# Kernel optimization log

Hardware: AMD Instinct MI355X
Metric: run time of the kernel (lower is better)

## Reference

```python
import jax, jax.numpy as jnp
import numpy as np
import math

MODEL_DIM = 1024
B, S = 4, 2048


def setup_inputs() -> dict:
    key = jax.random.key(0)
    k_x, k_q, k_k, k_v = jax.random.split(key, 4)
    r5 = math.sqrt(5)
    x = jax.random.normal(k_x, (B, S, MODEL_DIM), dtype=jnp.float32)
    Q = jax.random.uniform(k_q, (MODEL_DIM, MODEL_DIM), minval=-r5, maxval=r5, dtype=jnp.float32)
    K = jax.random.uniform(k_k, (MODEL_DIM, MODEL_DIM), minval=-r5, maxval=r5, dtype=jnp.float32)
    V = jax.random.uniform(k_v, (MODEL_DIM, MODEL_DIM), minval=-r5, maxval=r5, dtype=jnp.float32)
    # attention_input == 'both' -> a == model_dim -> F is the full identity
    F = jnp.eye(MODEL_DIM, dtype=jnp.float32)
    return {"x": x, "Q": Q, "K": K, "V": V, "F": F}


def reference(x, Q, K, V, F):
    d = x.shape[-1]
    xf = jnp.matmul(x, F)
    Qx = jnp.matmul(xf, Q)          # [B,S,D]
    Kx = jnp.matmul(xf, K)          # [B,S,D]
    Vx = jnp.matmul(x, V)           # [B,S,D]
    scores = jnp.einsum('bqd,bkd->bqk', Qx, Kx) / math.sqrt(d)  # [B,S,S]
    seq = x.shape[1]
    mask = jnp.triu(jnp.ones((seq, seq), dtype=bool), k=1)
    scores = jnp.where(mask, -jnp.inf, scores)
    probs = jax.nn.softmax(scores, axis=-1)
    out = jnp.matmul(probs, Vx)     # [B,S,D]
    return (out, probs)
```

## Files before the change

### kernel.cpp

```cpp
#include <hip/hip_runtime.h>
#include <hip/hip_fp16.h>

typedef _Float16 f16;
typedef __attribute__((ext_vector_type(8))) _Float16 f16x8;
typedef __attribute__((ext_vector_type(4))) _Float16 f16x4;
typedef __attribute__((ext_vector_type(4))) float    f32x4;

#define D_MODEL 1024
#define SEQ     2048
#define BATCH   4
#define M_TOT   (BATCH * SEQ)
#define NE      ((long)M_TOT * D_MODEL)
#define WE      ((long)D_MODEL * D_MODEL)
#define OUT_ELEMS  ((long)M_TOT * D_MODEL)

static __device__ __forceinline__ f16x8 frag_read(const f16* lds, int row, int c)
{
    const f16x8* L = (const f16x8*)lds;
    return L[row * 4 + (c ^ ((row >> 1) & 3))];
}

static __device__ __forceinline__ void stage_tile(const f16* __restrict__ g, int row0,
                                                  int ld, int k0, f16* ldsbase,
                                                  int wave, int lane)
{
#pragma unroll
    for (int j = 0; j < 2; ++j) {
        const int chunk = wave * 2 + j;
        const int off16 = chunk * 64 + lane;
        const int row   = off16 >> 2;
        const int slot  = (off16 & 3) ^ ((row >> 1) & 3);
        const f16* src = g + (long)(row0 + row) * ld + (k0 + slot * 8);
        f16* dst = ldsbase + chunk * 512;
        __builtin_amdgcn_global_load_lds((const __attribute__((address_space(1))) void*)src,
                                         (__attribute__((address_space(3))) void*)dst,
                                         16, 0, 0);
    }
}

template<int ROWS>
static __device__ __forceinline__ void stage8(const f16* __restrict__ g, int row0,
                                              int ld, int k0, f16* dstbase,
                                              int wave, int lane)
{
#pragma unroll
    for (int j = 0; j < ROWS / 128; ++j) {
        const int off16 = j * 512 + wave * 64 + lane;
        const int row   = off16 >> 2;
        const int slot  = (off16 & 3) ^ ((row >> 1) & 3);
        const f16* src = g + (long)(row0 + row) * ld + (k0 + slot * 8);
        f16* dst = dstbase + (j * 512 + wave * 64) * 8;
        __builtin_amdgcn_global_load_lds((const __attribute__((address_space(1))) void*)src,
                                         (__attribute__((address_space(3))) void*)dst,
                                         16, 0, 0);
    }
}

template<int DUAL> struct G8 {
    static constexpr int BUF    = DUAL ? 24576 : 12288;
    static constexpr int OFF_AL = 8192;
    static constexpr int OFF_BH = DUAL ? 16384 : 8192;
    static constexpr int OFF_BL = 20480;
};

template<int DUAL>
static __device__ __forceinline__ void g8_issueA(const f16* Ah, const f16* Al, int ld,
                                                 int m0, f16* lds, int t, int wave, int lane)
{
    f16* b = lds + (t & 1) * G8<DUAL>::BUF;
    stage8<256>(Ah, m0, ld, t * 32, b, wave, lane);
    if constexpr (DUAL) stage8<256>(Al, m0, ld, t * 32, b + G8<DUAL>::OFF_AL, wave, lane);
}
template<int DUAL>
static __device__ __forceinline__ void g8_issueBh(const f16* BTh, int ld, int n0,
                                                  f16* lds, int t, int wave, int lane)
{
    stage8<128>(BTh, n0, ld, t * 32, lds + (t & 1) * G8<DUAL>::BUF + G8<DUAL>::OFF_BH, wave, lane);
}
template<int DUAL>
static __device__ __forceinline__ void g8_issueBl(const f16* BTl, int ld, int n0,
                                                  f16* lds, int t, int wave, int lane)
{
    stage8<128>(BTl, n0, ld, t * 32, lds + (t & 1) * G8<DUAL>::BUF + G8<DUAL>::OFF_BL, wave, lane);
}

template<int DUAL>
static __device__ __forceinline__ void gemm8_pipe(
    const f16* __restrict__ Ah, const f16* __restrict__ Al,
    const f16* __restrict__ BTh, const f16* __restrict__ BTl,
    int ld, int m0, int n0, int nT, f16* lds, f32x4 acc[4][4], int wave, int lane)
{
    const int wr = wave >> 1, wc = wave & 1;
    const int cf = lane >> 4;

#pragma unroll
    for (int mi = 0; mi < 4; ++mi)
#pragma unroll
        for (int ni = 0; ni < 4; ++ni) acc[mi][ni] = (f32x4){0.f, 0.f, 0.f, 0.f};

    g8_issueA<DUAL>(Ah, Al, ld, m0, lds, 0, wave, lane);
    g8_issueBh<DUAL>(BTh, ld, n0, lds, 0, wave, lane);
    if constexpr (DUAL) g8_issueBl<DUAL>(BTl, ld, n0, lds, 0, wave, lane);
    g8_issueA<DUAL>(Ah, Al, ld, m0, lds, 1, wave, lane);
    g8_issueBh<DUAL>(BTh, ld, n0, lds, 1, wave, lane);

    for (int t = 0; t < nT; ++t) {
        if (t < nT - 1) {
            if constexpr (DUAL) {
                g8_issueBl<DUAL>(BTl, ld, n0, lds, t + 1, wave, lane);
                asm volatile("s_waitcnt vmcnt(6)" ::: "memory");
            } else {
                asm volatile("s_waitcnt vmcnt(3)" ::: "memory");
            }
        } else {
            asm volatile("s_waitcnt vmcnt(0)" ::: "memory");
        }
        __builtin_amdgcn_sched_barrier(0);
        __builtin_amdgcn_s_barrier();
        __builtin_amdgcn_sched_barrier(0);

        f16* buf = lds + (t & 1) * G8<DUAL>::BUF;

        f16x8 fbh[4], fbl[4];
#pragma unroll
        for (int i = 0; i < 4; ++i) {
            const int rb = wc * 64 + i * 16 + (lane & 15);
            fbh[i] = frag_read(buf + G8<DUAL>::OFF_BH, rb, cf);
            if constexpr (DUAL) fbl[i] = frag_read(buf + G8<DUAL>::OFF_BL, rb, cf);
        }
        f16x8 pah[2][2], pal[2][2];
#pragma unroll
        for (int j = 0; j < 2; ++j) {
            const int ra = wr * 64 + j * 16 + (lane & 15);
            pah[0][j] = frag_read(buf, ra, cf);
            if constexpr (DUAL) pal[0][j] = frag_read(buf + G8<DUAL>::OFF_AL, ra, cf);
        }
#pragma unroll
        for (int p = 0; p < 2; ++p) {
            const int cur = p & 1, nxt = cur ^ 1;
            if (p < 1) {
#pragma unroll
                for (int j = 0; j < 2; ++j) {
                    const int ra = wr * 64 + (2 * (p + 1) + j) * 16 + (lane & 15);
                    pah[nxt][j] = frag_read(buf, ra, cf);
                    if constexpr (DUAL) pal[nxt][j] = frag_read(buf + G8<DUAL>::OFF_AL, ra, cf);
                }
            }
            __builtin_amdgcn_s_setprio(1);
#pragma unroll
            for (int j = 0; j < 2; ++j)
#pragma unroll
                for (int ni = 0; ni < 4; ++ni)
                    acc[2 * p + j][ni] = __builtin_amdgcn_mfma_f32_16x16x32_f16(pah[cur][j], fbh[ni], acc[2 * p + j][ni], 0, 0, 0);
            if constexpr (DUAL) {
#pragma unroll
                for (int j = 0; j < 2; ++j)
#pragma unroll
                    for (int ni = 0; ni < 4; ++ni)
                        acc[2 * p + j][ni] = __builtin_amdgcn_mfma_f32_16x16x32_f16(pah[cur][j], fbl[ni], acc[2 * p + j][ni], 0, 0, 0);
#pragma unroll
                for (int j = 0; j < 2; ++j)
#pragma unroll
                    for (int ni = 0; ni < 4; ++ni)
                        acc[2 * p + j][ni] = __builtin_amdgcn_mfma_f32_16x16x32_f16(pal[cur][j], fbh[ni], acc[2 * p + j][ni], 0, 0, 0);
            }
            __builtin_amdgcn_s_setprio(0);
        }

        asm volatile("s_waitcnt lgkmcnt(0)" ::: "memory");
        __builtin_amdgcn_sched_barrier(0);
        __builtin_amdgcn_s_barrier();
        __builtin_amdgcn_sched_barrier(0);

        if (t < nT - 2) {
            g8_issueA<DUAL>(Ah, Al, ld, m0, lds, t + 2, wave, lane);
            g8_issueBh<DUAL>(BTh, ld, n0, lds, t + 2, wave, lane);
        }
        __builtin_amdgcn_sched_barrier(0);
    }
}

#define BUFE2 32768

static __device__ __forceinline__ void g256_main(const f16* Ah, const f16* Al,
                                                 const f16* BTh, int ld, int m0, int n0,
                                                 f16* lds, int t, int wave, int lane)
{
    f16* b = lds + (t & 1) * BUFE2;
    stage8<256>(Ah,  m0, ld, t * 32, b,         wave, lane);
    stage8<256>(Al,  m0, ld, t * 32, b + 8192,  wave, lane);
    stage8<256>(BTh, n0, ld, t * 32, b + 16384, wave, lane);
}
static __device__ __forceinline__ void g256_bl(const f16* BTl, int ld, int n0,
                                               f16* lds, int t, int wave, int lane)
{
    stage8<256>(BTl, n0, ld, t * 32, lds + (t & 1) * BUFE2 + 24576, wave, lane);
}

static __device__ __forceinline__ void gemm256d(
    const f16* __restrict__ Ah, const f16* __restrict__ Al,
    const f16* __restrict__ BTh, const f16* __restrict__ BTl,
    int ld, int m0, int n0, f16* lds, f32x4 acc[8][4], int wave, int lane)
{
    const int wr = wave >> 2, wc = wave & 3;
    const int cf = lane >> 4;

#pragma unroll
    for (int mi = 0; mi < 8; ++mi)
#pragma unroll
        for (int ni = 0; ni < 4; ++ni) acc[mi][ni] = (f32x4){0.f, 0.f, 0.f, 0.f};

    g256_main(Ah, Al, BTh, ld, m0, n0, lds, 0, wave, lane);
    g256_bl(BTl, ld, n0, lds, 0, wave, lane);
    g256_main(Ah, Al, BTh, ld, m0, n0, lds, 1, wave, lane);

    for (int t = 0; t < 32; ++t) {
        if (t < 31) {
            g256_bl(BTl, ld, n0, lds, t + 1, wave, lane);
            asm volatile("s_waitcnt vmcnt(8)" ::: "memory");
        } else {
            asm volatile("s_waitcnt vmcnt(0)" ::: "memory");
        }
        __builtin_amdgcn_sched_barrier(0);
        __builtin_amdgcn_s_barrier();
        __builtin_amdgcn_sched_barrier(0);

        f16* buf = lds + (t & 1) * BUFE2;

        f16x8 fbh[4], fbl[4];
#pragma unroll
        for (int ni = 0; ni < 4; ++ni) {
            const int rb = wc * 64 + ni * 16 + (lane & 15);
            fbh[ni] = frag_read(buf + 16384, rb, cf);
            fbl[ni] = frag_read(buf + 24576, rb, cf);
        }
        f16x8 pah[2][2], pal[2][2];
#pragma unroll
        for (int j = 0; j < 2; ++j) {
            const int ra = wr * 128 + j * 16 + (lane & 15);
            pah[0][j] = frag_read(buf,        ra, cf);
            pal[0][j] = frag_read(buf + 8192, ra, cf);
        }
#pragma unroll
        for (int p = 0; p < 4; ++p) {
            const int cur = p & 1, nxt = cur ^ 1;
            if (p < 3) {
#pragma unroll
                for (int j = 0; j < 2; ++j) {
                    const int ra = wr * 128 + (2 * (p + 1) + j) * 16 + (lane & 15);
                    pah[nxt][j] = frag_read(buf,        ra, cf);
                    pal[nxt][j] = frag_read(buf + 8192, ra, cf);
                }
            }
            __builtin_amdgcn_s_setprio(1);
#pragma unroll
            for (int j = 0; j < 2; ++j)
#pragma unroll
                for (int ni = 0; ni < 4; ++ni)
                    acc[2 * p + j][ni] = __builtin_amdgcn_mfma_f32_16x16x32_f16(pah[cur][j], fbh[ni], acc[2 * p + j][ni], 0, 0, 0);
#pragma unroll
            for (int j = 0; j < 2; ++j)
#pragma unroll
                for (int ni = 0; ni < 4; ++ni)
                    acc[2 * p + j][ni] = __builtin_amdgcn_mfma_f32_16x16x32_f16(pah[cur][j], fbl[ni], acc[2 * p + j][ni], 0, 0, 0);
#pragma unroll
            for (int j = 0; j < 2; ++j)
#pragma unroll
                for (int ni = 0; ni < 4; ++ni)
                    acc[2 * p + j][ni] = __builtin_amdgcn_mfma_f32_16x16x32_f16(pal[cur][j], fbh[ni], acc[2 * p + j][ni], 0, 0, 0);
            __builtin_amdgcn_s_setprio(0);
        }

        asm volatile("s_waitcnt lgkmcnt(0)" ::: "memory");
        __builtin_amdgcn_sched_barrier(0);
        __builtin_amdgcn_s_barrier();
        __builtin_amdgcn_sched_barrier(0);

        if (t < 30)
            g256_main(Ah, Al, BTh, ld, m0, n0, lds, t + 2, wave, lane);
        __builtin_amdgcn_sched_barrier(0);
    }
}

__global__ __launch_bounds__(512, 2) void k_gemm_T(
    const f16* __restrict__ xh, const f16* __restrict__ xl,
    const f16* __restrict__ WhT, const f16* __restrict__ WlT,
    f16* __restrict__ Th, f16* __restrict__ Tl)
{
    __shared__ __align__(16) f16 lds[49152];
    const int lane = threadIdx.x & 63, wave = threadIdx.x >> 6;
    const int L = blockIdx.x;
    const int swz = (L & 7) * 32 + (L >> 3);
    const int m0 = (swz >> 3) * 256;
    const int n0 = (swz & 7) * 128;
    f32x4 acc[4][4];
    gemm8_pipe<1>(xh, xl, WhT, WlT, D_MODEL, m0, n0, 32, lds, acc, wave, lane);
    const int wr = wave >> 1, wc = wave & 1;
#pragma unroll
    for (int mi = 0; mi < 4; ++mi)
#pragma unroll
        for (int ni = 0; ni < 4; ++ni) {
            const int gn = n0 + wc * 64 + ni * 16 + (lane & 15);
#pragma unroll
            for (int r = 0; r < 4; ++r) {
                const int gm = m0 + wr * 64 + mi * 16 + (lane >> 4) * 4 + r;
                const float v = acc[mi][ni][r];
                const f16 h = (f16)v;
                Th[(long)gm * D_MODEL + gn] = h;
                Tl[(long)gm * D_MODEL + gn] = (f16)(v - (float)h);
            }
        }
}

__global__ __launch_bounds__(512, 2) void k_mega1(
    const f16* __restrict__ Th, const f16* __restrict__ Tl,
    const f16* __restrict__ xh, const f16* __restrict__ xl,
    const f16* __restrict__ VhT,
    float* __restrict__ scores, f16* __restrict__ VxT)
{
    __shared__ __align__(16) f16 lds[65536];
    const int lane = threadIdx.x & 63, wave = threadIdx.x >> 6;

    if (blockIdx.x < 144) {
        const int L = blockIdx.x;
        const int b = L / 36;
        const int t = L - b * 36;
        int qt = (int)((sqrtf(8.f * (float)t + 1.f) - 1.f) * 0.5f);
        while ((qt + 1) * (qt + 2) / 2 <= t) ++qt;
        while (qt * (qt + 1) / 2 > t) --qt;
        const int kt = t - qt * (qt + 1) / 2;

        const long ob = (long)b * SEQ * D_MODEL;
        f32x4 acc[8][4];
        gemm256d(Th + ob, Tl + ob, xh + ob, xl + ob, D_MODEL,
                 qt * 256, kt * 256, lds, acc, wave, lane);

        float* sb = scores + (long)b * SEQ * SEQ;
        const int wr = wave >> 2, wc = wave & 3;
#pragma unroll
        for (int mi = 0; mi < 8; ++mi)
#pragma unroll
            for (int ni = 0; ni < 4; ++ni) {
                const int k = kt * 256 + wc * 64 + ni * 16 + (lane & 15);
#pragma unroll
                for (int r = 0; r < 4; ++r) {
                    const int q = qt * 256 + wr * 128 + mi * 16 + (lane >> 4) * 4 + r;
                    __builtin_nontemporal_store(acc[mi][ni][r] * 0.03125f,
                                                &sb[(long)q * SEQ + k]);
                }
            }
    } else {
        const int idx = blockIdx.x - 144;
        const int m0 = (idx >> 3) * 256;
        const int n0 = (idx & 7) * 128;
        f32x4 acc[4][4];
        gemm8_pipe<0>(xh, nullptr, VhT, nullptr, D_MODEL, m0, n0, 32, lds, acc, wave, lane);
        const int wr = wave >> 1, wc = wave & 1;
#pragma unroll
        for (int mi = 0; mi < 4; ++mi) {
            const int gm0 = m0 + wr * 64 + mi * 16 + (lane >> 4) * 4;
            const int b = gm0 >> 11, s = gm0 & 2047;
#pragma unroll
            for (int ni = 0; ni < 4; ++ni) {
                const int gn = n0 + wc * 64 + ni * 16 + (lane & 15);
                f16x4 p = {(f16)acc[mi][ni][0], (f16)acc[mi][ni][1],
                           (f16)acc[mi][ni][2], (f16)acc[mi][ni][3]};
                *(f16x4*)(VxT + ((long)b * D_MODEL + gn) * SEQ + s) = p;
            }
        }
    }
}

__global__ __launch_bounds__(512, 4) void k_gemm_pv8(
    const f16* __restrict__ P, const f16* __restrict__ VT, float* __restrict__ out)
{
    __shared__ __align__(16) f16 lds[24576];
    const int lane = threadIdx.x & 63, wave = threadIdx.x >> 6;
    const int i = blockIdx.x;
    const int qt = 7 - (i >> 5);
    const int dt = (i >> 2) & 7;
    const int b  = i & 3;
    const int nT = 8 * (qt + 1);
    f32x4 acc[4][4];
    const f16* Pb  = P  + (long)b * SEQ * SEQ;
    const f16* VTb = VT + (long)b * D_MODEL * SEQ;
    gemm8_pipe<0>(Pb, nullptr, VTb, nullptr, SEQ, qt * 256, dt * 128, nT, lds, acc, wave, lane);
    float* ob = out + (long)b * SEQ * D_MODEL;
    const int wr = wave >> 1, wc = wave & 1;
#pragma unroll
    for (int mi = 0; mi < 4; ++mi)
#pragma unroll
        for (int ni = 0; ni < 4; ++ni) {
            const int d = dt * 128 + wc * 64 + ni * 16 + (lane & 15);
#pragma unroll
            for (int r = 0; r < 4; ++r) {
                const int qq = qt * 256 + wr * 64 + mi * 16 + (lane >> 4) * 4 + r;
                ob[(long)qq * D_MODEL + d] = acc[mi][ni][r];
            }
        }
}

static __device__ __forceinline__ void gemm_core_dual(
    const f16* __restrict__ Ah, const f16* __restrict__ Al,
    const f16* __restrict__ BTh, const f16* __restrict__ BTl,
    int ld, int m0, int n0, int kEnd, f16* lds, f32x4 acc[4][4])
{
    const int t = threadIdx.x;
    const int lane = t & 63;
    const int wave = t >> 6;
    const int wr = wave >> 1, wc = wave & 1;
    const int cfrag = lane >> 4;

#pragma unroll
    for (int mi = 0; mi < 4; ++mi)
#pragma unroll
        for (int ni = 0; ni < 4; ++ni)
            acc[mi][ni] = (f32x4){0.f, 0.f, 0.f, 0.f};

    for (int k0 = 0; k0 < kEnd; k0 += 32) {
        stage_tile(Ah,  m0, ld, k0, lds,         wave, lane);
        stage_tile(BTh, n0, ld, k0, lds + 4096,  wave, lane);
        stage_tile(Al,  m0, ld, k0, lds + 8192,  wave, lane);
        stage_tile(BTl, n0, ld, k0, lds + 12288, wave, lane);
        __syncthreads();

        f16x8 fah[4], fbh[4], fal[4], fbl[4];
#pragma unroll
        for (int i = 0; i < 4; ++i) {
            fah[i] = frag_read(lds,         wr * 64 + i * 16 + (lane & 15), cfrag);
            fbh[i] = frag_read(lds + 4096,  wc * 64 + i * 16 + (lane & 15), cfrag);
            fal[i] = frag_read(lds + 8192,  wr * 64 + i * 16 + (lane & 15), cfrag);
            fbl[i] = frag_read(lds + 12288, wc * 64 + i * 16 + (lane & 15), cfrag);
        }
#pragma unroll
        for (int mi = 0; mi < 4; ++mi)
#pragma unroll
            for (int ni = 0; ni < 4; ++ni) {
                acc[mi][ni] = __builtin_amdgcn_mfma_f32_16x16x32_f16(fah[mi], fbh[ni], acc[mi][ni], 0, 0, 0);
                acc[mi][ni] = __builtin_amdgcn_mfma_f32_16x16x32_f16(fah[mi], fbl[ni], acc[mi][ni], 0, 0, 0);
                acc[mi][ni] = __builtin_amdgcn_mfma_f32_16x16x32_f16(fal[mi], fbh[ni], acc[mi][ni], 0, 0, 0);
            }
        __syncthreads();
    }
}

__global__ __launch_bounds__(256) void k_split_all(
    const float* __restrict__ x, const float* __restrict__ Q,
    const float* __restrict__ K, const float* __restrict__ V,
    f16* __restrict__ xh, f16* __restrict__ xl,
    f16* __restrict__ Qh, f16* __restrict__ Ql,
    f16* __restrict__ Kh, f16* __restrict__ Kl,
    f16* __restrict__ VhT)
{
    __shared__ float tile[32][33];
    const int bid = blockIdx.x;
    if (bid < 2560) {
        const float* src; f16 *dh, *dl; long base;
        if (bid < 2048)      { src = x; dh = xh; dl = xl; base = (long)bid * 4096; }
        else if (bid < 2304) { src = Q; dh = Qh; dl = Ql; base = (long)(bid - 2048) * 4096; }
        else                 { src = K; dh = Kh; dl = Kl; base = (long)(bid - 2304) * 4096; }
#pragma unroll
        for (int j = 0; j < 4; ++j) {
            const long i = base + (j * 256 + threadIdx.x) * 4;
            float4 v = *(const float4*)(src + i);
            f16 h0 = (f16)v.x, h1 = (f16)v.y, h2 = (f16)v.z, h3 = (f16)v.w;
            f16x4 hh = {h0, h1, h2, h3};
            f16x4 ll = {(f16)(v.x - (float)h0), (f16)(v.y - (float)h1),
                        (f16)(v.z - (float)h2), (f16)(v.w - (float)h3)};
            *(f16x4*)(dh + i) = hh;
            *(f16x4*)(dl + i) = ll;
        }
    } else {
        const int idx = bid - 2560;
        const int n0 = (idx & 31) * 32, k0 = (idx >> 5) * 32;
        const int c = threadIdx.x & 31, r8 = threadIdx.x >> 5;
#pragma unroll
        for (int i = 0; i < 4; ++i) {
            const int r = r8 + i * 8;
            tile[r][c] = V[(long)(k0 + r) * D_MODEL + n0 + c];
        }
        __syncthreads();
#pragma unroll
        for (int i = 0; i < 4; ++i) {
            const int r = r8 + i * 8;
            VhT[(long)(n0 + r) * D_MODEL + k0 + c] = (f16)tile[c][r];
        }
    }
}

__global__ __launch_bounds__(256, 2) void k_gemm_w(
    const f16* __restrict__ Qh, const f16* __restrict__ Ql,
    const f16* __restrict__ Kh, const f16* __restrict__ Kl,
    f16* __restrict__ WhT, f16* __restrict__ WlT)
{
    __shared__ __align__(16) f16 lds[16384];
    f32x4 acc[4][4];
    const int m0 = blockIdx.y * 128, n0 = blockIdx.x * 128;
    gemm_core_dual(Qh, Ql, Kh, Kl, D_MODEL, m0, n0, D_MODEL, lds, acc);
    const int lane = threadIdx.x & 63, wave = threadIdx.x >> 6;
    const int wr = wave >> 1, wc = wave & 1;
#pragma unroll
    for (int mi = 0; mi < 4; ++mi)
#pragma unroll
        for (int ni = 0; ni < 4; ++ni) {
            const int gn = n0 + wc * 64 + ni * 16 + (lane & 15);
#pragma unroll
            for (int r = 0; r < 4; ++r) {
                const int gm = m0 + wr * 64 + mi * 16 + (lane >> 4) * 4 + r;
                const float v = acc[mi][ni][r];
                const f16 h = (f16)v;
                WhT[(long)gn * D_MODEL + gm] = h;
                WlT[(long)gn * D_MODEL + gm] = (f16)(v - (float)h);
            }
        }
}

__global__ __launch_bounds__(256) void k_softmax(float* __restrict__ probs,
                                                 f16* __restrict__ probs16)
{
    const long row = blockIdx.x;
    const int q = (int)(row & (SEQ - 1));
    float* s = probs + row * SEQ;
    const int t = threadIdx.x;
    const int kb = t * 8;
    float v[8] = {0.f, 0.f, 0.f, 0.f, 0.f, 0.f, 0.f, 0.f};
    if (kb <= q) {
        float4 u0 = *(const float4*)(s + kb);
        float4 u1 = *(const float4*)(s + kb + 4);
        v[0] = u0.x; v[1] = u0.y; v[2] = u0.z; v[3] = u0.w;
        v[4] = u1.x; v[5] = u1.y; v[6] = u1.z; v[7] = u1.w;
    }
    float mx = -3.0e38f;
#pragma unroll
    for (int j = 0; j < 8; ++j) if (kb + j <= q) mx = fmaxf(mx, v[j]);
#pragma unroll
    for (int off = 32; off > 0; off >>= 1) mx = fmaxf(mx, __shfl_xor(mx, off, 64));
    __shared__ float redA[4], redB[4];
    const int lane = t & 63, wave = t >> 6;
    if (lane == 0) redA[wave] = mx;
    __syncthreads();
    mx = fmaxf(fmaxf(redA[0], redA[1]), fmaxf(redA[2], redA[3]));
    float e[8]; float sum = 0.f;
#pragma unroll
    for (int j = 0; j < 8; ++j) { e[j] = (kb + j <= q) ? __expf(v[j] - mx) : 0.f; sum += e[j]; }
#pragma unroll
    for (int off = 32; off > 0; off >>= 1) sum += __shfl_xor(sum, off, 64);
    if (lane == 0) redB[wave] = sum;
    __syncthreads();
    sum = (redB[0] + redB[1]) + (redB[2] + redB[3]);
    const float inv = 1.f / sum;
    f32x4 w0 = {e[0] * inv, e[1] * inv, e[2] * inv, e[3] * inv};
    f32x4 w1 = {e[4] * inv, e[5] * inv, e[6] * inv, e[7] * inv};
    __builtin_nontemporal_store(w0, (f32x4*)(s + kb));
    __builtin_nontemporal_store(w1, (f32x4*)(s + kb + 4));
    f16x8 p16 = {(f16)w0.x, (f16)w0.y, (f16)w0.z, (f16)w0.w,
                 (f16)w1.x, (f16)w1.y, (f16)w1.z, (f16)w1.w};
    *(f16x8*)(probs16 + row * SEQ + kb) = p16;
}

extern "C" void kernel_launch(void* const* d_in, const int* in_sizes, int n_in,
                              void* d_out, int out_size, void* d_ws, size_t ws_size,
                              hipStream_t stream)
{
    const float* x = (const float*)d_in[0];
    const float* Q = (const float*)d_in[1];
    const float* K = (const float*)d_in[2];
    const float* V = (const float*)d_in[3];

    float* out   = (float*)d_out;
    float* probs = out + OUT_ELEMS;

    f16* base = (f16*)d_ws;
    f16* xh   = base;
    f16* xl   = base + NE;
    f16* Th   = base + 2 * NE;
    f16* Tl   = base + 3 * NE;
    f16* VxT  = base + 4 * NE;
    f16* Qh   = base + 5 * NE;
    f16* Ql   = Qh + WE;
    f16* Kh   = Qh + 2 * WE;
    f16* Kl   = Qh + 3 * WE;
    f16* WhT  = Qh + 4 * WE;
    f16* WlT  = Qh + 5 * WE;
    f16* VhT  = Qh + 6 * WE;
    f16* probs16 = base + 2 * NE;

    k_split_all<<<3584, 256, 0, stream>>>(x, Q, K, V, xh, xl, Qh, Ql, Kh, Kl, VhT);
    k_gemm_w<<<dim3(8, 8), 256, 0, stream>>>(Qh, Ql, Kh, Kl, WhT, WlT);
    k_gemm_T<<<256, 512, 0, stream>>>(xh, xl, WhT, WlT, Th, Tl);
    k_mega1<<<400, 512, 0, stream>>>(Th, Tl, xh, xl, VhT, probs, VxT);
    k_softmax<<<8192, 256, 0, stream>>>(probs, probs16);
    k_gemm_pv8<<<256, 512, 0, stream>>>(probs16, VxT, out);
}
```

Baseline: 260.1 us.

## Preload all A fragments per k-step and interleave score/V tiles across XCDs

The inner MFMA loops now load every A fragment for the k-step up front instead of double-buffering pairs of fragments between MFMA groups. This removes interleaved LDS reads but raises VGPR pressure. The mega kernel's block-to-work mapping is also reordered: the first 256 block ids are spread by bid&7, so each XCD gets a balanced mix of causal score tiles of every query-row size plus Vx GEMM tiles. The remaining Vx tiles follow, which is meant to even out per-XCD load and the tail.

```diff
diff --git a/kernel.cpp b/kernel.cpp
--- a/kernel.cpp
+++ b/kernel.cpp
@@ -120,59 +120,42 @@
         __builtin_amdgcn_sched_barrier(0);
 
         f16* buf = lds + (t & 1) * G8<DUAL>::BUF;
-
-        f16x8 fbh[4], fbl[4];
+        f16x8 fbh[4], fbl[4], fah[4], fal[4];
 #pragma unroll
         for (int i = 0; i < 4; ++i) {
             const int rb = wc * 64 + i * 16 + (lane & 15);
             fbh[i] = frag_read(buf + G8<DUAL>::OFF_BH, rb, cf);
             if constexpr (DUAL) fbl[i] = frag_read(buf + G8<DUAL>::OFF_BL, rb, cf);
         }
-        f16x8 pah[2][2], pal[2][2];
-#pragma unroll
-        for (int j = 0; j < 2; ++j) {
-            const int ra = wr * 64 + j * 16 + (lane & 15);
-            pah[0][j] = frag_read(buf, ra, cf);
-            if constexpr (DUAL) pal[0][j] = frag_read(buf + G8<DUAL>::OFF_AL, ra, cf);
-        }
-#pragma unroll
-        for (int p = 0; p < 2; ++p) {
-            const int cur = p & 1, nxt = cur ^ 1;
-            if (p < 1) {
-#pragma unroll
-                for (int j = 0; j < 2; ++j) {
-                    const int ra = wr * 64 + (2 * (p + 1) + j) * 16 + (lane & 15);
-                    pah[nxt][j] = frag_read(buf, ra, cf);
-                    if constexpr (DUAL) pal[nxt][j] = frag_read(buf + G8<DUAL>::OFF_AL, ra, cf);
-                }
-            }
-            __builtin_amdgcn_s_setprio(1);
-#pragma unroll
-            for (int j = 0; j < 2; ++j)
+#pragma unroll
+        for (int i = 0; i < 4; ++i) {
+            const int ra = wr * 64 + i * 16 + (lane & 15);
+            fah[i] = frag_read(buf, ra, cf);
+            if constexpr (DUAL) fal[i] = frag_read(buf + G8<DUAL>::OFF_AL, ra, cf);
+        }
+        __builtin_amdgcn_s_setprio(1);
+#pragma unroll
+        for (int mi = 0; mi < 4; ++mi) {
+#pragma unroll
+            for (int ni = 0; ni < 4; ++ni)
+                acc[mi][ni] = __builtin_amdgcn_mfma_f32_16x16x32_f16(fah[mi], fbh[ni], acc[mi][ni], 0, 0, 0);
+            if constexpr (DUAL) {
 #pragma unroll
                 for (int ni = 0; ni < 4; ++ni)
-                    acc[2 * p + j][ni] = __builtin_amdgcn_mfma_f32_16x16x32_f16(pah[cur][j], fbh[ni], acc[2 * p + j][ni], 0, 0, 0);
-            if constexpr (DUAL) {
-#pragma unroll
-                for (int j = 0; j < 2; ++j)
-#pragma unroll
-                    for (int ni = 0; ni < 4; ++ni)
-                        acc[2 * p + j][ni] = __builtin_amdgcn_mfma_f32_16x16x32_f16(pah[cur][j], fbl[ni], acc[2 * p + j][ni], 0, 0, 0);
-#pragma unroll
-                for (int j = 0; j < 2; ++j)
-#pragma unroll
-                    for (int ni = 0; ni < 4; ++ni)
-                        acc[2 * p + j][ni] = __builtin_amdgcn_mfma_f32_16x16x32_f16(pal[cur][j], fbh[ni], acc[2 * p + j][ni], 0, 0, 0);
-            }
-            __builtin_amdgcn_s_setprio(0);
-        }
+                    acc[mi][ni] = __builtin_amdgcn_mfma_f32_16x16x32_f16(fah[mi], fbl[ni], acc[mi][ni], 0, 0, 0);
+#pragma unroll
+                for (int ni = 0; ni < 4; ++ni)
+                    acc[mi][ni] = __builtin_amdgcn_mfma_f32_16x16x32_f16(fal[mi], fbh[ni], acc[mi][ni], 0, 0, 0);
+            }
+        }
+        __builtin_amdgcn_s_setprio(0);
 
         asm volatile("s_waitcnt lgkmcnt(0)" ::: "memory");
         __builtin_amdgcn_sched_barrier(0);
         __builtin_amdgcn_s_barrier();
         __builtin_amdgcn_sched_barrier(0);
 
-        if (t < nT - 2) {
+        if (t + 2 < nT) {
             g8_issueA<DUAL>(Ah, Al, ld, m0, lds, t + 2, wave, lane);
             g8_issueBh<DUAL>(BTh, ld, n0, lds, t + 2, wave, lane);
         }
@@ -226,50 +209,33 @@
         __builtin_amdgcn_sched_barrier(0);
 
         f16* buf = lds + (t & 1) * BUFE2;
-
-        f16x8 fbh[4], fbl[4];
+        f16x8 fbh[4], fbl[4], fah[8], fal[8];
 #pragma unroll
         for (int ni = 0; ni < 4; ++ni) {
             const int rb = wc * 64 + ni * 16 + (lane & 15);
             fbh[ni] = frag_read(buf + 16384, rb, cf);
             fbl[ni] = frag_read(buf + 24576, rb, cf);
         }
-        f16x8 pah[2][2], pal[2][2];
-#pragma unroll
-        for (int j = 0; j < 2; ++j) {
-            const int ra = wr * 128 + j * 16 + (lane & 15);
-            pah[0][j] = frag_read(buf,        ra, cf);
-            pal[0][j] = frag_read(buf + 8192, ra, cf);
-        }
-#pragma unroll
-        for (int p = 0; p < 4; ++p) {
-            const int cur = p & 1, nxt = cur ^ 1;
-            if (p < 3) {
-#pragma unroll
-                for (int j = 0; j < 2; ++j) {
-                    const int ra = wr * 128 + (2 * (p + 1) + j) * 16 + (lane & 15);
-                    pah[nxt][j] = frag_read(buf,        ra, cf);
-                    pal[nxt][j] = frag_read(buf + 8192, ra, cf);
-                }
-            }
-            __builtin_amdgcn_s_setprio(1);
-#pragma unroll
-            for (int j = 0; j < 2; ++j)
-#pragma unroll
-                for (int ni = 0; ni < 4; ++ni)
-                    acc[2 * p + j][ni] = __builtin_amdgcn_mfma_f32_16x16x32_f16(pah[cur][j], fbh[ni], acc[2 * p + j][ni], 0, 0, 0);
-#pragma unroll
-            for (int j = 0; j < 2; ++j)
-#pragma unroll
-                for (int ni = 0; ni < 4; ++ni)
-                    acc[2 * p + j][ni] = __builtin_amdgcn_mfma_f32_16x16x32_f16(pah[cur][j], fbl[ni], acc[2 * p + j][ni], 0, 0, 0);
-#pragma unroll
-            for (int j = 0; j < 2; ++j)
-#pragma unroll
-                for (int ni = 0; ni < 4; ++ni)
-                    acc[2 * p + j][ni] = __builtin_amdgcn_mfma_f32_16x16x32_f16(pal[cur][j], fbh[ni], acc[2 * p + j][ni], 0, 0, 0);
-            __builtin_amdgcn_s_setprio(0);
-        }
+#pragma unroll
+        for (int mi = 0; mi < 8; ++mi) {
+            const int ra = wr * 128 + mi * 16 + (lane & 15);
+            fah[mi] = frag_read(buf,        ra, cf);
+            fal[mi] = frag_read(buf + 8192, ra, cf);
+        }
+        __builtin_amdgcn_s_setprio(1);
+#pragma unroll
+        for (int mi = 0; mi < 8; ++mi) {
+#pragma unroll
+            for (int ni = 0; ni < 4; ++ni)
+                acc[mi][ni] = __builtin_amdgcn_mfma_f32_16x16x32_f16(fah[mi], fbh[ni], acc[mi][ni], 0, 0, 0);
+#pragma unroll
+            for (int ni = 0; ni < 4; ++ni)
+                acc[mi][ni] = __builtin_amdgcn_mfma_f32_16x16x32_f16(fah[mi], fbl[ni], acc[mi][ni], 0, 0, 0);
+#pragma unroll
+            for (int ni = 0; ni < 4; ++ni)
+                acc[mi][ni] = __builtin_amdgcn_mfma_f32_16x16x32_f16(fal[mi], fbh[ni], acc[mi][ni], 0, 0, 0);
+        }
+        __builtin_amdgcn_s_setprio(0);
 
         asm volatile("s_waitcnt lgkmcnt(0)" ::: "memory");
         __builtin_amdgcn_sched_barrier(0);
@@ -320,39 +286,40 @@
 {
     __shared__ __align__(16) f16 lds[65536];
     const int lane = threadIdx.x & 63, wave = threadIdx.x >> 6;
-
-    if (blockIdx.x < 144) {
-        const int L = blockIdx.x;
-        const int b = L / 36;
-        const int t = L - b * 36;
-        int qt = (int)((sqrtf(8.f * (float)t + 1.f) - 1.f) * 0.5f);
-        while ((qt + 1) * (qt + 2) / 2 <= t) ++qt;
-        while (qt * (qt + 1) / 2 > t) --qt;
-        const int kt = t - qt * (qt + 1) / 2;
-
-        const long ob = (long)b * SEQ * D_MODEL;
+    const int bid = blockIdx.x;
+
+    int s_qt = -1, s_b = 0, s_kt = 0, vidx = -1;
+    if (bid < 256) {
+        const int x = bid & 7;
+        const int slot = bid >> 3;
+        const int cx = 4 * (x + 1);
+        if (slot < cx) { s_qt = x; s_b = slot / (x + 1); s_kt = slot % (x + 1); }
+        else           { vidx = 32 * x - 2 * x * (x + 1) + (slot - cx); }
+    } else vidx = 112 + (bid - 256);
+
+    if (s_qt >= 0) {
+        const long ob = (long)s_b * SEQ * D_MODEL;
         f32x4 acc[8][4];
         gemm256d(Th + ob, Tl + ob, xh + ob, xl + ob, D_MODEL,
-                 qt * 256, kt * 256, lds, acc, wave, lane);
-
-        float* sb = scores + (long)b * SEQ * SEQ;
+                 s_qt * 256, s_kt * 256, lds, acc, wave, lane);
+
+        float* sb = scores + (long)s_b * SEQ * SEQ;
         const int wr = wave >> 2, wc = wave & 3;
 #pragma unroll
         for (int mi = 0; mi < 8; ++mi)
 #pragma unroll
             for (int ni = 0; ni < 4; ++ni) {
-                const int k = kt * 256 + wc * 64 + ni * 16 + (lane & 15);
+                const int k = s_kt * 256 + wc * 64 + ni * 16 + (lane & 15);
 #pragma unroll
                 for (int r = 0; r < 4; ++r) {
-                    const int q = qt * 256 + wr * 128 + mi * 16 + (lane >> 4) * 4 + r;
+                    const int q = s_qt * 256 + wr * 128 + mi * 16 + (lane >> 4) * 4 + r;
                     __builtin_nontemporal_store(acc[mi][ni][r] * 0.03125f,
                                                 &sb[(long)q * SEQ + k]);
                 }
             }
     } else {
-        const int idx = blockIdx.x - 144;
-        const int m0 = (idx >> 3) * 256;
-        const int n0 = (idx & 7) * 128;
+        const int m0 = (vidx >> 3) * 256;
+        const int n0 = (vidx & 7) * 128;
         f32x4 acc[4][4];
         gemm8_pipe<0>(xh, nullptr, VhT, nullptr, D_MODEL, m0, n0, 32, lds, acc, wave, lane);
         const int wr = wave >> 1, wc = wave & 1;
```

New measurement: 281.6 us. +8.3%, slower.
